# Optimization experiments

Hardware: AMD Instinct MI355X
Metric: run time of the kernel (lower is better)

The kernel has to match this reference:

```python
import jax, jax.numpy as jnp
import numpy as np

B, N, C_IN, L, C_OUT = 8, 50000, 32, 9, 64
M, NNZ = 12500, 37500


def setup_inputs() -> dict:
    key = jax.random.key(0)
    k = jax.random.split(key, 7)
    x = jax.random.normal(k[0], (B, N, C_IN), dtype=jnp.float32)
    weight = jax.random.normal(k[1], (L * C_IN, C_OUT), dtype=jnp.float32) * (1.0 / np.sqrt(L * C_IN))
    bias = jax.random.normal(k[2], (C_OUT,), dtype=jnp.float32) * 0.01
    values = jax.random.uniform(k[3], (NNZ,), dtype=jnp.float32)
    spiral_indices = jax.random.randint(k[4], (N, L), 0, N, dtype=jnp.int64)
    rows = jax.random.randint(k[5], (NNZ,), 0, M, dtype=jnp.int64)
    cols = jax.random.randint(k[6], (NNZ,), 0, N, dtype=jnp.int64)
    return {"x": x, "weight": weight, "bias": bias, "values": values,
            "spiral_indices": spiral_indices, "rows": rows, "cols": cols,
            "num_out_verts": M}


def reference(x, weight, bias, values, spiral_indices, rows, cols, num_out_verts):
    b, n, c = x.shape
    # SpiralConv: gather spiral neighborhoods, flatten, linear
    g = x[:, spiral_indices]                      # [B, N, L, C]
    g = g.reshape(b, n, -1)                       # [B, N, L*C]
    out = jnp.einsum('bnk,ko->bno', g, weight) + bias
    out = jax.nn.elu(out)                         # [B, N, C_OUT]
    # Pool: sparse down_transform (gather, scale, scatter_add)
    gathered = out[:, cols] * values[None, :, None]          # [B, NNZ, C_OUT]
    pooled = jnp.zeros((b, num_out_verts, out.shape[-1]), dtype=out.dtype)
    pooled = pooled.at[:, rows].add(gathered)                # [B, M, C_OUT]
    return pooled
```

## Files before the change

### kernel.cpp

```cpp
#include <hip/hip_runtime.h>

#define BATCH   8
#define NVERT   50000
#define CIN     32
#define LSP     9
#define COUT    64
#define MVERT   12500
#define NNZ     37500

#define TILE_T  64
#define TPB     586
#define NFRAG   2304
#define OUTDW   (BATCH * MVERT * COUT)
#define XELEMS  (BATCH * NVERT * CIN)

#define PRE_BLOCKS  6250
#define PACK_BLOCKS 9
#define ZERO_BLOCKS 6250
#define HZ_BLOCKS   49

typedef __attribute__((ext_vector_type(8))) short  short8;
typedef __attribute__((ext_vector_type(4))) float  floatx4;

static __device__ __forceinline__ unsigned short f2bf(float f) {
    union { float f; unsigned int u; } c; c.f = f;
    unsigned int u = c.u;
    return (unsigned short)((u + 0x7fffu + ((u >> 16) & 1u)) >> 16);
}

static __device__ __forceinline__ void dma16(const void* g, void* l) {
    typedef __attribute__((address_space(1))) const void gvoid;
    typedef __attribute__((address_space(3))) void lvoid;
    __builtin_amdgcn_global_load_lds(
        (gvoid*)(unsigned long long)g,
        (lvoid*)(unsigned int)(unsigned long long)l,
        16, 0, 0);
}

__global__ __launch_bounds__(256)
void prep_kernel(const float* __restrict__ x, const float* __restrict__ w,
                 unsigned short* __restrict__ x16, unsigned short* __restrict__ wp,
                 float* __restrict__ out, int* __restrict__ hist)
{
    const int blk = blockIdx.x;
    const int tid = threadIdx.x;
    if (blk < PRE_BLOCKS) {
        const size_t base = ((size_t)blk * 256 + tid) * 8;
        const float4* s = (const float4*)(x + base);
        float4 a = s[0], c = s[1];
        unsigned short t[8];
        t[0]=f2bf(a.x); t[1]=f2bf(a.y); t[2]=f2bf(a.z); t[3]=f2bf(a.w);
        t[4]=f2bf(c.x); t[5]=f2bf(c.y); t[6]=f2bf(c.z); t[7]=f2bf(c.w);
        *(uint4*)(x16 + base) = *(uint4*)t;
    } else if (blk < PRE_BLOCKS + PACK_BLOCKS) {
        const int f = (blk - PRE_BLOCKS) * 256 + tid;
        if (f < NFRAG) {
            int s = f >> 8, g = (f >> 6) & 3, lane = f & 63;
            int k0 = s * 32 + (lane >> 4) * 8, col = g * 16 + (lane & 15);
            unsigned short t[8];
            #pragma unroll
            for (int j = 0; j < 8; ++j)
                t[j] = f2bf(w[(size_t)(k0 + j) * COUT + col]);
            ((uint4*)wp)[f] = *(uint4*)t;
        }
    } else if (blk < PRE_BLOCKS + PACK_BLOCKS + ZERO_BLOCKS) {
        const size_t base = ((size_t)(blk - PRE_BLOCKS - PACK_BLOCKS) * 256 + tid) * 4;
        if (base < OUTDW) *(uint4*)(out + base) = (uint4){0, 0, 0, 0};
    } else {
        const int i = (blk - PRE_BLOCKS - PACK_BLOCKS - ZERO_BLOCKS) * 256 + tid;
        if (i < MVERT) hist[i] = 0;
    }
}

__global__ __launch_bounds__(256)
void hist_kernel(const int* __restrict__ rows, int* __restrict__ hist) {
    int z = blockIdx.x * 256 + threadIdx.x;
    if (z < NNZ) atomicAdd(&hist[rows[z]], 1);
}

__global__ __launch_bounds__(1024)
void scan_kernel(const int* __restrict__ hist, int* __restrict__ off2) {
    __shared__ int sh[1024];
    const int t = threadIdx.x;
    const int base = t * 13;
    int loc[13];
    int s = 0;
    #pragma unroll
    for (int j = 0; j < 13; ++j) {
        int i = base + j;
        int v = (i < MVERT) ? hist[i] : 0;
        loc[j] = s; s += v;
    }
    sh[t] = s;
    __syncthreads();
    for (int d = 1; d < 1024; d <<= 1) {
        int v = (t >= d) ? sh[t - d] : 0;
        __syncthreads();
        sh[t] += v;
        __syncthreads();
    }
    const int excl = sh[t] - s;
    #pragma unroll
    for (int j = 0; j < 13; ++j) {
        int i = base + j;
        if (i < MVERT) off2[i] = excl + loc[j];
    }
}

__global__ __launch_bounds__(256)
void scatter_kernel(const int* __restrict__ rows, const int* __restrict__ cols,
                    const float* __restrict__ vals, int* __restrict__ off2,
                    int* __restrict__ rows_s, int* __restrict__ cols_s,
                    float* __restrict__ vals_s) {
    int z = blockIdx.x * 256 + threadIdx.x;
    if (z < NNZ) {
        int r = rows[z];
        int pos = atomicAdd(&off2[r], 1);
        rows_s[pos] = r;
        cols_s[pos] = cols[z];
        vals_s[pos] = vals[z];
    }
}

__global__ __launch_bounds__(256)
void spiral_mfma3_kernel(const unsigned short* __restrict__ x16,
                         const unsigned short* __restrict__ wp,
                         const float* __restrict__ bias,
                         const int* __restrict__ spiral,
                         const int* __restrict__ rows_s,
                         const int* __restrict__ cols_s,
                         const float* __restrict__ vals_s,
                         float* __restrict__ out)
{
    __shared__ unsigned short sG[4 * 4608];

    const int bid  = blockIdx.x;
    const int b    = bid / TPB;
    const int tile = bid - b * TPB;
    const int z0   = tile * TILE_T;
    const int tcnt = min(TILE_T, NNZ - z0);
    const int tid  = threadIdx.x;
    const int w    = tid >> 6;
    const int lane = tid & 63;
    const int quad = lane >> 4;
    const int m16  = lane & 15;
    const int z0w  = z0 + 16 * w;
    int nval = tcnt - 16 * w;
    nval = (nval < 0) ? 0 : ((nval > 16) ? 16 : nval);

    unsigned short* region = sG + w * 4608;

    const int zc    = min(z0w + m16, NNZ - 1);
    const int c     = cols_s[zc];
    const int myrow = rows_s[zc];
    const int* sp   = spiral + c * LSP;

    const unsigned short* xb = x16 + (size_t)b * NVERT * CIN;
    #pragma unroll
    for (int s = 0; s < 9; ++s) {
        int idx = sp[s];
        dma16(xb + (size_t)idx * CIN + quad * 8, region + s * 512);
    }
    asm volatile("s_waitcnt vmcnt(0)" ::: "memory");

    floatx4 acc[4];
    #pragma unroll
    for (int g = 0; g < 4; ++g) acc[g] = (floatx4){0.f, 0.f, 0.f, 0.f};

    #pragma unroll
    for (int s = 0; s < 9; ++s) {
        short8 af = *(const short8*)(region + s * 512 + quad * 128 + m16 * 8);
        #pragma unroll
        for (int g = 0; g < 4; ++g) {
            short8 bf = *(const short8*)(wp + (size_t)((s * 4 + g) * 64 + lane) * 8);
            acc[g] = __builtin_amdgcn_mfma_f32_16x16x32_bf16(af, bf, acc[g], 0, 0, 0);
        }
    }

    if (nval > 0) {
        float bs[4];
        #pragma unroll
        for (int g = 0; g < 4; ++g) bs[g] = bias[g * 16 + m16];
        float vr[4];
        #pragma unroll
        for (int r = 0; r < 4; ++r) vr[r] = vals_s[min(z0w + quad * 4 + r, NNZ - 1)];

        #pragma unroll
        for (int r = 0; r < 4; ++r) {
            const int tt = quad * 4 + r;
            #pragma unroll
            for (int g = 0; g < 4; ++g) {
                float y = acc[g][r] + bs[g];
                y = (y > 0.0f) ? y : (__expf(y) - 1.0f);
                *(float*)((char*)region + tt * 256 + (g * 16 + m16) * 4) = y * vr[r];
            }
        }

        const int ch = lane;
        float a = 0.0f;
        int cur = __shfl(myrow, 0, 16);
        for (int t = 0; t < nval; ++t) {
            int rt = __shfl(myrow, t, 16);
            if (rt != cur) {
                atomicAdd(out + ((size_t)b * MVERT + cur) * COUT + ch, a);
                a = 0.0f; cur = rt;
            }
            a += *(const float*)((char*)region + t * 256 + ch * 4);
        }
        atomicAdd(out + ((size_t)b * MVERT + cur) * COUT + ch, a);
    }
}

extern "C" void kernel_launch(void* const* d_in, const int* in_sizes, int n_in,
                              void* d_out, int out_size, void* d_ws, size_t ws_size,
                              hipStream_t stream) {
    const float* x      = (const float*)d_in[0];
    const float* w      = (const float*)d_in[1];
    const float* bias   = (const float*)d_in[2];
    const float* vals   = (const float*)d_in[3];
    const int*   spiral = (const int*)d_in[4];
    const int*   rows   = (const int*)d_in[5];
    const int*   cols   = (const int*)d_in[6];
    float* out = (float*)d_out;

    char* base = (char*)d_ws;
    unsigned short* wp     = (unsigned short*)(base);
    unsigned short* x16    = (unsigned short*)(base + 36864);
    int*            hist   = (int*)(base + 25636864);
    int*            off2   = (int*)(base + 25686864);
    int*            rows_s = (int*)(base + 25736864);
    int*            cols_s = (int*)(base + 25886880);
    float*          vals_s = (float*)(base + 26036896);

    const int prep_grid = PRE_BLOCKS + PACK_BLOCKS + ZERO_BLOCKS + HZ_BLOCKS;
    prep_kernel<<<prep_grid, 256, 0, stream>>>(x, w, x16, wp, out, hist);
    hist_kernel<<<147, 256, 0, stream>>>(rows, hist);
    scan_kernel<<<1, 1024, 0, stream>>>(hist, off2);
    scatter_kernel<<<147, 256, 0, stream>>>(rows, cols, vals, off2,
                                            rows_s, cols_s, vals_s);
    spiral_mfma3_kernel<<<BATCH * TPB, 256, 0, stream>>>(x16, wp, bias, spiral,
                                                         rows_s, cols_s, vals_s, out);
}
```

Baseline: 185.0 us.

## Process 64 nonzeros per wave with direct register gathers and batch-interleaved tiles

Each wave now handles four 16-row MFMA tiles (64 nonzeros) instead of one, so each weight fragment loaded per spiral step is reused across four tiles. The LDS DMA staging of gathered x rows is dropped; A fragments are loaded straight from global memory using spiral indices shared across lanes with shuffles. Block indexing puts the batch in the low bits so neighbouring blocks share a tile and reuse spiral/column data in cache. In exchange, register pressure is higher (64 accumulator floats per lane), the grid has four times fewer blocks, and the per-tile scatter epilogue runs serially.

Result: faster. 179.5 us (-3.0%).

```diff
diff --git a/kernel.cpp b/kernel.cpp
--- a/kernel.cpp
+++ b/kernel.cpp
@@ -8,8 +8,8 @@
 #define MVERT   12500
 #define NNZ     37500
 
-#define TILE_T  64
-#define TPB     586
+#define TILE_T  256
+#define TPB     147
 #define NFRAG   2304
 #define OUTDW   (BATCH * MVERT * COUT)
 #define XELEMS  (BATCH * NVERT * CIN)
@@ -26,15 +26,6 @@
     union { float f; unsigned int u; } c; c.f = f;
     unsigned int u = c.u;
     return (unsigned short)((u + 0x7fffu + ((u >> 16) & 1u)) >> 16);
-}
-
-static __device__ __forceinline__ void dma16(const void* g, void* l) {
-    typedef __attribute__((address_space(1))) const void gvoid;
-    typedef __attribute__((address_space(3))) void lvoid;
-    __builtin_amdgcn_global_load_lds(
-        (gvoid*)(unsigned long long)g,
-        (lvoid*)(unsigned int)(unsigned long long)l,
-        16, 0, 0);
 }
 
 __global__ __launch_bounds__(256)
@@ -123,7 +114,7 @@
 }
 
 __global__ __launch_bounds__(256)
-void spiral_mfma3_kernel(const unsigned short* __restrict__ x16,
+void spiral_mfma4_kernel(const unsigned short* __restrict__ x16,
                          const unsigned short* __restrict__ wp,
                          const float* __restrict__ bias,
                          const int* __restrict__ spiral,
@@ -132,82 +123,88 @@
                          const float* __restrict__ vals_s,
                          float* __restrict__ out)
 {
-    __shared__ unsigned short sG[4 * 4608];
+    __shared__ float sS[4 * 16 * 68];
 
     const int bid  = blockIdx.x;
-    const int b    = bid / TPB;
-    const int tile = bid - b * TPB;
-    const int z0   = tile * TILE_T;
-    const int tcnt = min(TILE_T, NNZ - z0);
+    const int b    = bid & 7;
+    const int tile = bid >> 3;
     const int tid  = threadIdx.x;
     const int w    = tid >> 6;
     const int lane = tid & 63;
     const int quad = lane >> 4;
     const int m16  = lane & 15;
-    const int z0w  = z0 + 16 * w;
-    int nval = tcnt - 16 * w;
-    nval = (nval < 0) ? 0 : ((nval > 16) ? 16 : nval);
-
-    unsigned short* region = sG + w * 4608;
-
-    const int zc    = min(z0w + m16, NNZ - 1);
-    const int c     = cols_s[zc];
-    const int myrow = rows_s[zc];
-    const int* sp   = spiral + c * LSP;
+    const int z0w  = tile * TILE_T + 64 * w;
+
+    const int   zc   = min(z0w + lane, NNZ - 1);
+    const int   colv = cols_s[zc];
+    const int   rowv = rows_s[zc];
+    const float valv = vals_s[zc];
+
+    int idx[9];
+    #pragma unroll
+    for (int s = 0; s < 9; ++s) idx[s] = spiral[colv * LSP + s];
 
     const unsigned short* xb = x16 + (size_t)b * NVERT * CIN;
+
+    floatx4 acc[4][4];
+    #pragma unroll
+    for (int mt = 0; mt < 4; ++mt)
+        #pragma unroll
+        for (int g = 0; g < 4; ++g) acc[mt][g] = (floatx4){0.f, 0.f, 0.f, 0.f};
+
     #pragma unroll
     for (int s = 0; s < 9; ++s) {
-        int idx = sp[s];
-        dma16(xb + (size_t)idx * CIN + quad * 8, region + s * 512);
-    }
-    asm volatile("s_waitcnt vmcnt(0)" ::: "memory");
-
-    floatx4 acc[4];
-    #pragma unroll
-    for (int g = 0; g < 4; ++g) acc[g] = (floatx4){0.f, 0.f, 0.f, 0.f};
-
-    #pragma unroll
-    for (int s = 0; s < 9; ++s) {
-        short8 af = *(const short8*)(region + s * 512 + quad * 128 + m16 * 8);
-        #pragma unroll
-        for (int g = 0; g < 4; ++g) {
-            short8 bf = *(const short8*)(wp + (size_t)((s * 4 + g) * 64 + lane) * 8);
-            acc[g] = __builtin_amdgcn_mfma_f32_16x16x32_bf16(af, bf, acc[g], 0, 0, 0);
-        }
-    }
-
-    if (nval > 0) {
-        float bs[4];
-        #pragma unroll
-        for (int g = 0; g < 4; ++g) bs[g] = bias[g * 16 + m16];
-        float vr[4];
-        #pragma unroll
-        for (int r = 0; r < 4; ++r) vr[r] = vals_s[min(z0w + quad * 4 + r, NNZ - 1)];
+        short8 bf[4];
+        #pragma unroll
+        for (int g = 0; g < 4; ++g)
+            bf[g] = *(const short8*)(wp + (size_t)((s * 4 + g) * 64 + lane) * 8);
+        #pragma unroll
+        for (int mt = 0; mt < 4; ++mt) {
+            int tix = __shfl(idx[s], mt * 16 + m16);
+            short8 af = *(const short8*)(xb + (size_t)tix * CIN + quad * 8);
+            #pragma unroll
+            for (int g = 0; g < 4; ++g)
+                acc[mt][g] = __builtin_amdgcn_mfma_f32_16x16x32_bf16(af, bf[g], acc[mt][g], 0, 0, 0);
+        }
+    }
+
+    float* region = sS + w * (16 * 68);
+    float bs[4];
+    #pragma unroll
+    for (int g = 0; g < 4; ++g) bs[g] = bias[g * 16 + m16];
+
+    float* outb = out + (size_t)b * MVERT * COUT;
+
+    #pragma unroll
+    for (int mt = 0; mt < 4; ++mt) {
+        const int zbase = z0w + mt * 16;
+        int nval = NNZ - zbase;
+        nval = (nval < 0) ? 0 : ((nval > 16) ? 16 : nval);
+        if (nval <= 0) continue;
 
         #pragma unroll
         for (int r = 0; r < 4; ++r) {
             const int tt = quad * 4 + r;
+            const float vv = __shfl(valv, mt * 16 + tt);
             #pragma unroll
             for (int g = 0; g < 4; ++g) {
-                float y = acc[g][r] + bs[g];
+                float y = acc[mt][g][r] + bs[g];
                 y = (y > 0.0f) ? y : (__expf(y) - 1.0f);
-                *(float*)((char*)region + tt * 256 + (g * 16 + m16) * 4) = y * vr[r];
+                region[tt * 68 + g * 16 + m16] = y * vv;
             }
         }
 
-        const int ch = lane;
         float a = 0.0f;
-        int cur = __shfl(myrow, 0, 16);
+        int cur = __shfl(rowv, mt * 16);
         for (int t = 0; t < nval; ++t) {
-            int rt = __shfl(myrow, t, 16);
+            int rt = __shfl(rowv, mt * 16 + t);
             if (rt != cur) {
-                atomicAdd(out + ((size_t)b * MVERT + cur) * COUT + ch, a);
+                atomicAdd(outb + (size_t)cur * COUT + lane, a);
                 a = 0.0f; cur = rt;
             }
-            a += *(const float*)((char*)region + t * 256 + ch * 4);
-        }
-        atomicAdd(out + ((size_t)b * MVERT + cur) * COUT + ch, a);
+            a += region[t * 68 + lane];
+        }
+        atomicAdd(outb + (size_t)cur * COUT + lane, a);
     }
 }
 
@@ -238,6 +235,6 @@
     scan_kernel<<<1, 1024, 0, stream>>>(hist, off2);
     scatter_kernel<<<147, 256, 0, stream>>>(rows, cols, vals, off2,
                                             rows_s, cols_s, vals_s);
-    spiral_mfma3_kernel<<<BATCH * TPB, 256, 0, stream>>>(x16, wp, bias, spiral,
+    spiral_mfma4_kernel<<<BATCH * TPB, 256, 0, stream>>>(x16, wp, bias, spiral,
                                                          rows_s, cols_s, vals_s, out);
 }
```
